# Performance work log

Hardware: AMD Instinct MI355X
Metric: run time of the kernel (lower is better)

## Reference

```python
import jax, jax.numpy as jnp
import numpy as np

HEADS = 4
PLANES = 256
IN_PLANES = 1024
W = H = D = 14
N = W * H * D  # 2744 tokens
EPS = 1e-5


def _bn_train(x, g, b):
    # training-mode BatchNorm3d: stats over (batch, spatial)
    mean = x.mean(axis=(0, 2, 3, 4), keepdims=True)
    var = ((x - mean) ** 2).mean(axis=(0, 2, 3, 4), keepdims=True)
    return g.reshape(1, -1, 1, 1, 1) * (x - mean) / jnp.sqrt(var + EPS) + b.reshape(1, -1, 1, 1, 1)


def _conv1x1(Wm, x):
    # 1x1x1 conv == channel matmul
    return jnp.einsum('oc,bcwhd->bowhd', Wm, x)


def setup_inputs() -> dict:
    key = jax.random.key(0)
    ks = jax.random.split(key, 16)
    dh = PLANES // HEADS
    s1 = 1.0 / np.sqrt(IN_PLANES)
    s2 = 1.0 / np.sqrt(PLANES)
    return {
        'x': jax.random.normal(ks[0], (4, IN_PLANES, W, H, D), jnp.float32),
        'W1': jax.random.uniform(ks[1], (PLANES, IN_PLANES), jnp.float32, -s1, s1),
        'g1': jnp.ones((PLANES,), jnp.float32),
        'b1': jnp.zeros((PLANES,), jnp.float32),
        'Wq': jax.random.uniform(ks[2], (PLANES, PLANES), jnp.float32, -s2, s2),
        'bq': jax.random.uniform(ks[3], (PLANES,), jnp.float32, -s2, s2),
        'Wk': jax.random.uniform(ks[4], (PLANES, PLANES), jnp.float32, -s2, s2),
        'bk': jax.random.uniform(ks[5], (PLANES,), jnp.float32, -s2, s2),
        'Wv': jax.random.uniform(ks[6], (PLANES, PLANES), jnp.float32, -s2, s2),
        'bv': jax.random.uniform(ks[7], (PLANES,), jnp.float32, -s2, s2),
        'rel_h': jax.random.normal(ks[8], (1, HEADS, dh, 1, H, D), jnp.float32),
        'rel_w': jax.random.normal(ks[9], (1, HEADS, dh, W, 1, D), jnp.float32),
        'rel_d': jax.random.normal(ks[10], (1, HEADS, dh, W, H, 1), jnp.float32),
        'g2': jnp.ones((PLANES,), jnp.float32),
        'b2': jnp.zeros((PLANES,), jnp.float32),
        'W3': jax.random.uniform(ks[11], (PLANES * 4, PLANES), jnp.float32, -s2, s2),
        'g3': jnp.ones((PLANES * 4,), jnp.float32),
        'b3': jnp.zeros((PLANES * 4,), jnp.float32),
    }


def _mhsa(x, Wq, bq, Wk, bk, Wv, bv, rel_h, rel_w, rel_d):
    B, C = x.shape[0], x.shape[1]
    dh = C // HEADS
    def proj(Wm, bm):
        y = _conv1x1(Wm, x) + bm.reshape(1, -1, 1, 1, 1)
        return y.reshape(B, HEADS, dh, N)
    q = proj(Wq, bq)
    k = proj(Wk, bk)
    v = proj(Wv, bv)
    # content-content: q^T k -> [B, H, N, N]
    cc = jnp.einsum('bhdn,bhdm->bhnm', q, k)
    # relative position term: (rel_h+rel_w+rel_d) broadcast to [1,H,dh,W,H,D]
    rel = (rel_h + rel_w + rel_d).reshape(HEADS, dh, N)
    cp = jnp.einsum('hdn,bhdm->bhnm', rel, q)
    attn = jax.nn.softmax(cc + cp, axis=-1)
    # out[...,n] = sum_m v[...,m] * attn[n, m]
    out = jnp.einsum('bhdm,bhnm->bhdn', v, attn)
    return out.reshape(B, C, W, H, D)


def reference(x, W1, g1, b1, Wq, bq, Wk, bk, Wv, bv, rel_h, rel_w, rel_d, g2, b2, W3, g3, b3):
    residual = x
    out = jax.nn.relu(_bn_train(_conv1x1(W1, x), g1, b1))
    out = _mhsa(out, Wq, bq, Wk, bk, Wv, bv, rel_h, rel_w, rel_d)
    out = jax.nn.relu(_bn_train(out, g2, b2))
    out = _bn_train(_conv1x1(W3, out), g3, b3)
    out = jax.nn.relu(out + residual)
    return out
```

## Files before the change

### kernel.cpp

```cpp
#include <hip/hip_runtime.h>
#include <hip/hip_bf16.h>
#include <math.h>

#define B_ 4
#define C1 1024
#define C2 256
#define HEADS_ 4
#define N_ 2744
#define NT_ 10976
#define EPS_ 1e-5f

typedef float f32x4 __attribute__((ext_vector_type(4)));
typedef short bf16x8 __attribute__((ext_vector_type(8)));
typedef unsigned short us4 __attribute__((ext_vector_type(4)));

static __device__ __forceinline__ unsigned short bfbits(float x) {
    __hip_bfloat16 t = __float2bfloat16(x);
    unsigned short u; __builtin_memcpy(&u, &t, 2); return u;
}

__global__ __launch_bounds__(256) void prep(
    const float* __restrict__ W1, const float* __restrict__ Wq, const float* __restrict__ Wk,
    const float* __restrict__ Wv, const float* __restrict__ W3,
    unsigned short* __restrict__ Wb, float* __restrict__ sums)
{
    const int bidx = blockIdx.x, t = threadIdx.x;
    if (bidx < 704) {
        const int i0 = (bidx * 256 + t) * 4;
        const float* src; int off;
        if (i0 < 262144)      { src = W1; off = i0; }
        else if (i0 < 327680) { src = Wq; off = i0 - 262144; }
        else if (i0 < 393216) { src = Wk; off = i0 - 327680; }
        else if (i0 < 458752) { src = Wv; off = i0 - 393216; }
        else                  { src = W3; off = i0 - 458752; }
        const float4 v = *(const float4*)&src[off];
        us4 pk; pk[0] = bfbits(v.x); pk[1] = bfbits(v.y); pk[2] = bfbits(v.z); pk[3] = bfbits(v.w);
        *(us4*)&Wb[i0] = pk;
    } else {
        float4 z; z.x = z.y = z.z = z.w = 0.f;
        *(float4*)&sums[t * 4] = z;
    }
}

__global__ __launch_bounds__(256) void xt_kernel(const float* __restrict__ x,
                                                 unsigned short* __restrict__ xT)
{
    __shared__ float ld[64][65];
    const int b = blockIdx.z, c0 = blockIdx.y << 6, n0 = blockIdx.x << 6;
    const int t = threadIdx.x, tn = t & 63, tg = t >> 6;
    const int gn = n0 + tn;
#pragma unroll
    for (int i = 0; i < 16; ++i) {
        const int c = tg * 16 + i;
        ld[c][tn] = (gn < N_) ? x[((size_t)b * C1 + c0 + c) * N_ + gn] : 0.f;
    }
    __syncthreads();
#pragma unroll
    for (int i = 0; i < 16; ++i) {
        const int n = tg * 16 + i;
        if (n0 + n < N_)
            xT[((size_t)b * N_ + n0 + n) * C1 + c0 + tn] = bfbits(ld[tn][n]);
    }
}

__global__ __launch_bounds__(256, 4) void gemm_nt(
    const unsigned short* __restrict__ A, const unsigned short* __restrict__ Bm,
    const float* __restrict__ bias, void* __restrict__ out0, void* __restrict__ out1,
    int M, int NC, int K, long aStride, long bStride, long oStride, int ldc, int mode)
{
    __shared__ char smem[24576];
    const int z = blockIdx.z;
    const int row0 = blockIdx.x << 7;
    const int col0 = blockIdx.y << 6;
    const unsigned short* Ag = A + (size_t)z * aStride;
    const unsigned short* Bg = Bm + (size_t)z * bStride;
    const int t = threadIdx.x;
    const int wave = t >> 6, lane = t & 63, l4 = lane >> 4, l15 = lane & 15;
    const int wr0 = wave << 5;

    f32x4 acc[2][4];
#pragma unroll
    for (int mi = 0; mi < 2; ++mi)
#pragma unroll
        for (int ks = 0; ks < 4; ++ks) acc[mi][ks] = (f32x4){0.f, 0.f, 0.f, 0.f};

    const int nk = K >> 6;
    for (int kt = 0; kt < nk; ++kt) {
        const int k0 = kt << 6;
        __syncthreads();
#pragma unroll
        for (int c = 0; c < 4; ++c) {
            const int e = c * 256 + t;
            const int r = e >> 3, ke = (e & 7) << 3;
            const int gr = min(row0 + r, M - 1);
            const bf16x8 v = *(const bf16x8*)(Ag + (size_t)gr * K + k0 + ke);
            *(bf16x8*)&smem[r * 128 + ((ke * 2) ^ ((r & 7) << 4))] = v;
        }
#pragma unroll
        for (int c = 0; c < 2; ++c) {
            const int e = c * 256 + t;
            const int r = e >> 3, ke = (e & 7) << 3;
            const int gr = min(col0 + r, NC - 1);
            const bf16x8 v = *(const bf16x8*)(Bg + (size_t)gr * K + k0 + ke);
            *(bf16x8*)&smem[16384 + r * 128 + ((ke * 2) ^ ((r & 7) << 4))] = v;
        }
        __syncthreads();
#pragma unroll
        for (int kc = 0; kc < 2; ++kc) {
            const int colb = kc * 64 + l4 * 16;
            const int ra0 = wr0 + l15, ra1 = wr0 + 16 + l15;
            const bf16x8 a0 = *(const bf16x8*)&smem[ra0 * 128 + (colb ^ ((ra0 & 7) << 4))];
            const bf16x8 a1 = *(const bf16x8*)&smem[ra1 * 128 + (colb ^ ((ra1 & 7) << 4))];
#pragma unroll
            for (int ks = 0; ks < 4; ++ks) {
                const int rb = ks * 16 + l15;
                const bf16x8 bf = *(const bf16x8*)&smem[16384 + rb * 128 + (colb ^ ((rb & 7) << 4))];
                acc[0][ks] = __builtin_amdgcn_mfma_f32_16x16x32_bf16(a0, bf, acc[0][ks], 0, 0, 0);
                acc[1][ks] = __builtin_amdgcn_mfma_f32_16x16x32_bf16(a1, bf, acc[1][ks], 0, 0, 0);
            }
        }
    }

    if (mode == 0) {
        float* o0 = (float*)out0 + (size_t)z * oStride;
#pragma unroll
        for (int mi = 0; mi < 2; ++mi)
#pragma unroll
            for (int ks = 0; ks < 4; ++ks)
#pragma unroll
                for (int j = 0; j < 4; ++j) {
                    const int row = row0 + wr0 + mi * 16 + l4 * 4 + j;
                    const int col = col0 + ks * 16 + l15;
                    if (row < M && col < NC) o0[(size_t)row * ldc + col] = acc[mi][ks][j];
                }
    } else if (mode == 3) {
        unsigned short* o0 = (unsigned short*)out0;
#pragma unroll
        for (int mi = 0; mi < 2; ++mi)
#pragma unroll
            for (int ks = 0; ks < 4; ++ks)
#pragma unroll
                for (int j = 0; j < 4; ++j) {
                    const int row = row0 + wr0 + mi * 16 + l4 * 4 + j;
                    const int col = col0 + ks * 16 + l15;
                    if (row < M && col < NC)
                        o0[((size_t)z * C2 + row) * N_ + col] = bfbits(acc[mi][ks][j] + bias[row]);
                }
    } else {
        unsigned short* yq = (unsigned short*)out0;
        unsigned short* yk = (unsigned short*)out1;
        const int h = col0 >> 6;
        const size_t bhbase = (size_t)(z * HEADS_ + h) * N_;
#pragma unroll
        for (int mi = 0; mi < 2; ++mi)
#pragma unroll
            for (int ks = 0; ks < 4; ++ks) {
                const int dcol = ks * 16 + l15;
                const float bvl = bias[col0 + dcol];
#pragma unroll
                for (int j = 0; j < 4; ++j) {
                    const int row = row0 + wr0 + mi * 16 + l4 * 4 + j;
                    if (row >= M) continue;
                    const unsigned short pv = bfbits(acc[mi][ks][j] + bvl);
                    if (mode == 1) {
                        yq[(bhbase + row) * 128 + dcol] = pv;
                        yk[(bhbase + row) * 128 + 64 + dcol] = pv;
                    } else {
                        yq[(bhbase + row) * 128 + dcol] = pv;
                    }
                }
            }
    }
}

__global__ __launch_bounds__(256) void bn_stats_t(const float* __restrict__ Y,
                                                  float* __restrict__ sums)
{
    const int c = threadIdx.x;
    float s = 0.f, s2 = 0.f;
    for (int row = blockIdx.x; row < NT_; row += gridDim.x) {
        const float v = Y[(size_t)row * 256 + c];
        s += v; s2 += v * v;
    }
    atomicAdd(&sums[c], s);
    atomicAdd(&sums[256 + c], s2);
}

__global__ __launch_bounds__(256) void bn_finalize_t(const float* __restrict__ sums,
    const float* __restrict__ g, const float* __restrict__ bb, float* __restrict__ scsh)
{
    const int c = threadIdx.x;
    const float m = sums[c] * (1.f / NT_);
    const float var = sums[256 + c] * (1.f / NT_) - m * m;
    const float istd = rsqrtf(var + EPS_);
    const float sc = g[c] * istd;
    scsh[c] = sc;
    scsh[256 + c] = bb[c] - m * sc;
}

__global__ __launch_bounds__(256) void bn_apply_t(const float* __restrict__ Y,
    const float* __restrict__ scsh, unsigned short* __restrict__ Yb)
{
    const int total4 = NT_ * 256 / 4;
    for (int i4 = blockIdx.x * 256 + threadIdx.x; i4 < total4; i4 += gridDim.x * 256) {
        const int i = i4 << 2;
        const int c0 = i & 255;
        const float4 v = *(const float4*)&Y[i];
        const float4 sc = *(const float4*)&scsh[c0];
        const float4 sh = *(const float4*)&scsh[256 + c0];
        us4 pk;
        pk[0] = bfbits(fmaxf(fmaf(v.x, sc.x, sh.x), 0.f));
        pk[1] = bfbits(fmaxf(fmaf(v.y, sc.y, sh.y), 0.f));
        pk[2] = bfbits(fmaxf(fmaf(v.z, sc.z, sh.z), 0.f));
        pk[3] = bfbits(fmaxf(fmaf(v.w, sc.w, sh.w), 0.f));
        *(us4*)&Yb[i] = pk;
    }
}

__global__ __launch_bounds__(256) void rel_fill(
    const float* __restrict__ rh, const float* __restrict__ rw, const float* __restrict__ rd,
    unsigned short* __restrict__ QAt)
{
    const int idx = blockIdx.x * 256 + threadIdx.x;
    if (idx >= HEADS_ * 16 * N_) return;
    const int n = idx % N_;
    const int t2 = idx / N_;
    const int h = t2 >> 4, dq = t2 & 15;
    const int dd = n % 14;
    const int hh = (n / 14) % 14;
    const int w = n / 196;
    us4 pk;
#pragma unroll
    for (int i = 0; i < 4; ++i) {
        const int base = (h * 64 + dq * 4 + i) * 196;
        const float v = rh[base + hh * 14 + dd]
                      + rw[base + w * 14 + dd]
                      + rd[base + w * 14 + hh];
        pk[i] = bfbits(v);
    }
#pragma unroll
    for (int b = 0; b < B_; ++b)
        *(us4*)&QAt[((size_t)(b * HEADS_ + h) * N_ + n) * 128 + 64 + dq * 4] = pk;
}

#define ALQ 0
#define ALK 32768
#define ALP 49152

__global__ __launch_bounds__(256, 2) void attn_mfma(
    const unsigned short* __restrict__ QAt, const unsigned short* __restrict__ KBt,
    const unsigned short* __restrict__ Vb, float* __restrict__ Ot)
{
    __shared__ char smem[65536];
    const int bid = blockIdx.x;
    const int sw = (bid & 7) * 44 + (bid >> 3);
    const int bh = sw / 22;
    const int ntile = sw - bh * 22;
    const int n0 = ntile << 7;
    const int b = bh >> 2, h = bh & 3;

    const unsigned short* qat = QAt + (size_t)bh * N_ * 128;
    const unsigned short* kbt = KBt + (size_t)bh * N_ * 128;
    const unsigned short* vb  = Vb + (size_t)(b * C2 + h * 64) * N_;
    float* ot = Ot + (size_t)b * N_ * 256 + h * 64;

    const int t = threadIdx.x;
    const int wave = t >> 6, lane = t & 63, l4 = lane >> 4, l15 = lane & 15;
    const int wq0 = wave << 5;

#pragma unroll
    for (int c = 0; c < 8; ++c) {
        const int o = (c * 256 + t) * 16;
        const int q = o >> 8, cb = o & 255;
        const int gq = min(n0 + q, N_ - 1);
        const bf16x8 v = *(const bf16x8*)(qat + (size_t)gq * 128 + (cb >> 1));
        *(bf16x8*)&smem[ALQ + q * 256 + (cb ^ ((q & 7) << 4))] = v;
    }

    float m_r[2][4], l_r[2][4];
    f32x4 oacc[2][4];
#pragma unroll
    for (int mi = 0; mi < 2; ++mi)
#pragma unroll
        for (int j = 0; j < 4; ++j) { m_r[mi][j] = -1e30f; l_r[mi][j] = 0.f; }
#pragma unroll
    for (int mi = 0; mi < 2; ++mi)
#pragma unroll
        for (int ds = 0; ds < 4; ++ds) oacc[mi][ds] = (f32x4){0.f, 0.f, 0.f, 0.f};

    for (int kt = 0; kt < 43; ++kt) {
        const int m0 = kt << 6;
#pragma unroll
        for (int c = 0; c < 4; ++c) {
            const int o = (c * 256 + t) * 16;
            const int r = o >> 8, cb = o & 255;
            const int gm = min(m0 + r, N_ - 1);
            const bf16x8 v = *(const bf16x8*)(kbt + (size_t)gm * 128 + (cb >> 1));
            *(bf16x8*)&smem[ALK + r * 256 + (cb ^ ((r & 7) << 4))] = v;
        }
        __syncthreads();
        bf16x8 bvr[2][4];
#pragma unroll
        for (int mc = 0; mc < 2; ++mc)
#pragma unroll
            for (int ds = 0; ds < 4; ++ds) {
                const int ms = min(m0 + mc * 32 + l4 * 8, N_ - 8);
                bvr[mc][ds] = *(const bf16x8*)(vb + (size_t)(ds * 16 + l15) * N_ + ms);
            }
        f32x4 s[2][4];
#pragma unroll
        for (int mi = 0; mi < 2; ++mi)
#pragma unroll
            for (int ks = 0; ks < 4; ++ks) s[mi][ks] = (f32x4){0.f, 0.f, 0.f, 0.f};
#pragma unroll
        for (int kc = 0; kc < 4; ++kc) {
            const int colb = kc * 64 + l4 * 16;
            const int q0r = wq0 + l15;
            const int q1r = wq0 + 16 + l15;
            const bf16x8 a0 = *(const bf16x8*)&smem[ALQ + q0r * 256 + (colb ^ ((q0r & 7) << 4))];
            const bf16x8 a1 = *(const bf16x8*)&smem[ALQ + q1r * 256 + (colb ^ ((q1r & 7) << 4))];
#pragma unroll
            for (int ks = 0; ks < 4; ++ks) {
                const int r = ks * 16 + l15;
                const bf16x8 bf = *(const bf16x8*)&smem[ALK + r * 256 + (colb ^ ((r & 7) << 4))];
                s[0][ks] = __builtin_amdgcn_mfma_f32_16x16x32_bf16(a0, bf, s[0][ks], 0, 0, 0);
                s[1][ks] = __builtin_amdgcn_mfma_f32_16x16x32_bf16(a1, bf, s[1][ks], 0, 0, 0);
            }
        }
        if (m0 + 64 > N_) {
#pragma unroll
            for (int ks = 0; ks < 4; ++ks)
                if (m0 + ks * 16 + l15 >= N_) {
                    s[0][ks] = (f32x4){-1e30f, -1e30f, -1e30f, -1e30f};
                    s[1][ks] = (f32x4){-1e30f, -1e30f, -1e30f, -1e30f};
                }
        }
        const int pbase = ALP + (wave << 12);
#pragma unroll
        for (int mi = 0; mi < 2; ++mi) {
#pragma unroll
            for (int j = 0; j < 4; ++j) {
                const float v0 = s[mi][0][j], v1 = s[mi][1][j];
                const float v2 = s[mi][2][j], v3 = s[mi][3][j];
                float rmax = fmaxf(fmaxf(v0, v1), fmaxf(v2, v3));
                rmax = fmaxf(rmax, __shfl_xor(rmax, 1, 64));
                rmax = fmaxf(rmax, __shfl_xor(rmax, 2, 64));
                rmax = fmaxf(rmax, __shfl_xor(rmax, 4, 64));
                rmax = fmaxf(rmax, __shfl_xor(rmax, 8, 64));
                const float mnew = fmaxf(m_r[mi][j], rmax);
                const float p0 = __expf(v0 - mnew), p1 = __expf(v1 - mnew);
                const float p2 = __expf(v2 - mnew), p3 = __expf(v3 - mnew);
                float ps = p0 + p1 + p2 + p3;
                ps += __shfl_xor(ps, 1, 64);
                ps += __shfl_xor(ps, 2, 64);
                ps += __shfl_xor(ps, 4, 64);
                ps += __shfl_xor(ps, 8, 64);
                const float scl = __expf(m_r[mi][j] - mnew);
                m_r[mi][j] = mnew;
                l_r[mi][j] = l_r[mi][j] * scl + ps;
                oacc[mi][0][j] *= scl; oacc[mi][1][j] *= scl;
                oacc[mi][2][j] *= scl; oacc[mi][3][j] *= scl;
                const int r = mi * 16 + l4 * 4 + j;
                const int rb = pbase + r * 128, sz = (r & 7) << 4;
                *(unsigned short*)&smem[rb + ((l15 * 2 +  0) ^ sz)] = bfbits(p0);
                *(unsigned short*)&smem[rb + ((l15 * 2 + 32) ^ sz)] = bfbits(p1);
                *(unsigned short*)&smem[rb + ((l15 * 2 + 64) ^ sz)] = bfbits(p2);
                *(unsigned short*)&smem[rb + ((l15 * 2 + 96) ^ sz)] = bfbits(p3);
            }
        }
#pragma unroll
        for (int mc = 0; mc < 2; ++mc) {
            const int colb = mc * 64 + l4 * 16;
            const int r0 = l15, r1 = 16 + l15;
            const bf16x8 pa0 = *(const bf16x8*)&smem[pbase + r0 * 128 + (colb ^ ((r0 & 7) << 4))];
            const bf16x8 pa1 = *(const bf16x8*)&smem[pbase + r1 * 128 + (colb ^ ((r1 & 7) << 4))];
#pragma unroll
            for (int ds = 0; ds < 4; ++ds) {
                oacc[0][ds] = __builtin_amdgcn_mfma_f32_16x16x32_bf16(pa0, bvr[mc][ds], oacc[0][ds], 0, 0, 0);
                oacc[1][ds] = __builtin_amdgcn_mfma_f32_16x16x32_bf16(pa1, bvr[mc][ds], oacc[1][ds], 0, 0, 0);
            }
        }
        __syncthreads();
    }

#pragma unroll
    for (int mi = 0; mi < 2; ++mi)
#pragma unroll
        for (int j = 0; j < 4; ++j) {
            const int n = n0 + wq0 + mi * 16 + l4 * 4 + j;
            if (n < N_) {
                const float inv = 1.f / l_r[mi][j];
#pragma unroll
                for (int ds = 0; ds < 4; ++ds)
                    ot[(size_t)n * 256 + ds * 16 + l15] = oacc[mi][ds][j] * inv;
            }
        }
}

__global__ __launch_bounds__(256) void bn_stats(const float* __restrict__ Y,
                                                float* __restrict__ mean, float* __restrict__ istd,
                                                int Cch)
{
    const int ch = blockIdx.x;
    float s = 0.f, s2 = 0.f;
    for (int i = threadIdx.x; i < NT_; i += 256) {
        const int b = i / N_, n = i - b * N_;
        const float v = Y[((size_t)b * Cch + ch) * N_ + n];
        s += v; s2 += v * v;
    }
#pragma unroll
    for (int off = 32; off > 0; off >>= 1) {
        s  += __shfl_down(s, off, 64);
        s2 += __shfl_down(s2, off, 64);
    }
    __shared__ float red[8];
    const int wid = threadIdx.x >> 6;
    if ((threadIdx.x & 63) == 0) { red[wid] = s; red[4 + wid] = s2; }
    __syncthreads();
    if (threadIdx.x == 0) {
        s = red[0] + red[1] + red[2] + red[3];
        s2 = red[4] + red[5] + red[6] + red[7];
        const float m = s / (float)NT_;
        const float var = s2 / (float)NT_ - m * m;
        mean[ch] = m;
        istd[ch] = rsqrtf(var + EPS_);
    }
}

__global__ __launch_bounds__(256) void bn_add_relu(float* __restrict__ Y, const float* __restrict__ X,
    const float* __restrict__ g, const float* __restrict__ bt,
    const float* __restrict__ mean, const float* __restrict__ istd)
{
    const int total4 = B_ * C1 * (N_ / 4);
    for (int i4 = blockIdx.x * 256 + threadIdx.x; i4 < total4; i4 += gridDim.x * 256) {
        const int i = i4 << 2;
        const int ch = (i / N_) % C1;
        const float sc = g[ch] * istd[ch];
        const float sh = bt[ch] - mean[ch] * sc;
        float4 y = *(float4*)&Y[i];
        const float4 x = *(const float4*)&X[i];
        y.x = fmaxf(fmaf(y.x, sc, sh) + x.x, 0.f);
        y.y = fmaxf(fmaf(y.y, sc, sh) + x.y, 0.f);
        y.z = fmaxf(fmaf(y.z, sc, sh) + x.z, 0.f);
        y.w = fmaxf(fmaf(y.w, sc, sh) + x.w, 0.f);
        *(float4*)&Y[i] = y;
    }
}

extern "C" void kernel_launch(void* const* d_in, const int* in_sizes, int n_in,
                              void* d_out, int out_size, void* d_ws, size_t ws_size,
                              hipStream_t stream)
{
    const float* x  = (const float*)d_in[0];
    const float* W1 = (const float*)d_in[1];
    const float* g1 = (const float*)d_in[2];
    const float* b1 = (const float*)d_in[3];
    const float* Wq = (const float*)d_in[4];
    const float* bq = (const float*)d_in[5];
    const float* Wk = (const float*)d_in[6];
    const float* bk = (const float*)d_in[7];
    const float* Wv = (const float*)d_in[8];
    const float* bv = (const float*)d_in[9];
    const float* rh = (const float*)d_in[10];
    const float* rw = (const float*)d_in[11];
    const float* rd = (const float*)d_in[12];
    const float* g2 = (const float*)d_in[13];
    const float* b2 = (const float*)d_in[14];
    const float* W3 = (const float*)d_in[15];
    const float* g3 = (const float*)d_in[16];
    const float* b3 = (const float*)d_in[17];
    float* out = (float*)d_out;

    float* ws = (float*)d_ws;
    unsigned short* xT  = (unsigned short*)ws;
    unsigned short* QAt = (unsigned short*)ws;
    unsigned short* KBt = (unsigned short*)(ws + 2809856);
    float* Y1t = ws + 5619712;
    float* Ot  = Y1t;
    unsigned short* Y1t16 = (unsigned short*)(ws + 8429568);
    unsigned short* Obt16 = Y1t16;
    unsigned short* Vb16 = (unsigned short*)(ws + 9834496);
    unsigned short* Wb = (unsigned short*)(ws + 11239424);
    unsigned short* W1b = Wb;
    unsigned short* Wqb = Wb + 262144;
    unsigned short* Wkb = Wb + 327680;
    unsigned short* Wvb = Wb + 393216;
    unsigned short* W3b = Wb + 458752;
    float* st = ws + 11599872;
    float* sums1 = st;
    float* sums2 = st + 512;
    float* scsh1 = st + 1024;
    float* scsh2 = st + 1536;
    float* m3 = st + 2048;
    float* i3 = st + 3072;

    dim3 blk(256);

    prep<<<dim3(705), blk, 0, stream>>>(W1, Wq, Wk, Wv, W3, Wb, sums1);
    xt_kernel<<<dim3(43, 16, B_), blk, 0, stream>>>(x, xT);

    gemm_nt<<<dim3(22, 4, B_), blk, 0, stream>>>(xT, W1b, nullptr, Y1t, nullptr,
        N_, 256, 1024, (long)N_ * 1024, 0, (long)N_ * 256, 256, 0);
    bn_stats_t<<<dim3(128), blk, 0, stream>>>(Y1t, sums1);
    bn_finalize_t<<<dim3(1), blk, 0, stream>>>(sums1, g1, b1, scsh1);
    bn_apply_t<<<dim3(1024), blk, 0, stream>>>(Y1t, scsh1, Y1t16);

    rel_fill<<<dim3((HEADS_ * 16 * N_ + 255) / 256), blk, 0, stream>>>(rh, rw, rd, QAt);

    gemm_nt<<<dim3(22, 4, B_), blk, 0, stream>>>(Y1t16, Wqb, bq, QAt, KBt,
        N_, 256, 256, (long)N_ * 256, 0, 0, 0, 1);
    gemm_nt<<<dim3(22, 4, B_), blk, 0, stream>>>(Y1t16, Wkb, bk, KBt, nullptr,
        N_, 256, 256, (long)N_ * 256, 0, 0, 0, 2);
    gemm_nt<<<dim3(2, 43, B_), blk, 0, stream>>>(Wvb, Y1t16, bv, Vb16, nullptr,
        256, N_, 256, 0, (long)N_ * 256, 0, 0, 3);

    attn_mfma<<<dim3(352), blk, 0, stream>>>(QAt, KBt, Vb16, Ot);

    bn_stats_t<<<dim3(128), blk, 0, stream>>>(Ot, sums2);
    bn_finalize_t<<<dim3(1), blk, 0, stream>>>(sums2, g2, b2, scsh2);
    bn_apply_t<<<dim3(1024), blk, 0, stream>>>(Ot, scsh2, Obt16);

    gemm_nt<<<dim3(8, 43, B_), blk, 0, stream>>>(W3b, Obt16, nullptr, out, nullptr,
        1024, N_, 256, 0, (long)N_ * 256, (long)C1 * N_, N_, 0);
    bn_stats<<<dim3(C1), blk, 0, stream>>>(out, m3, i3, C1);
    bn_add_relu<<<dim3(2048), blk, 0, stream>>>(out, x, g3, b3, m3, i3);

    (void)in_sizes; (void)n_in; (void)out_size; (void)ws_size;
}
```

Before: 497.5 us.

## Halve attention query tile to double blocks and fuse Q/K projection GEMMs

The attention kernel now processes 64 query rows per block instead of 128: each wave owns 16 rows, shared memory shrinks to 40KB and launch bounds allow 4 blocks per CU, so 688 blocks launch instead of 352. This is meant to improve occupancy and fill the 256 CUs, at the cost of each block reloading K and V tiles twice as often. Separately, the Q and K projection GEMMs are merged into a single launch over a concatenated 512-column weight, picking the bias and output buffer by column range. This removes one launch and rereads of the activation input.

```diff
diff --git a/kernel.cpp b/kernel.cpp
--- a/kernel.cpp
+++ b/kernel.cpp
@@ -65,7 +65,8 @@
 
 __global__ __launch_bounds__(256, 4) void gemm_nt(
     const unsigned short* __restrict__ A, const unsigned short* __restrict__ Bm,
-    const float* __restrict__ bias, void* __restrict__ out0, void* __restrict__ out1,
+    const float* __restrict__ bias0, const float* __restrict__ bias1,
+    void* __restrict__ out0, void* __restrict__ out1,
     int M, int NC, int K, long aStride, long bStride, long oStride, int ldc, int mode)
 {
     __shared__ char smem[24576];
@@ -144,29 +145,31 @@
                     const int row = row0 + wr0 + mi * 16 + l4 * 4 + j;
                     const int col = col0 + ks * 16 + l15;
                     if (row < M && col < NC)
-                        o0[((size_t)z * C2 + row) * N_ + col] = bfbits(acc[mi][ks][j] + bias[row]);
+                        o0[((size_t)z * C2 + row) * N_ + col] = bfbits(acc[mi][ks][j] + bias0[row]);
                 }
     } else {
         unsigned short* yq = (unsigned short*)out0;
         unsigned short* yk = (unsigned short*)out1;
-        const int h = col0 >> 6;
-        const size_t bhbase = (size_t)(z * HEADS_ + h) * N_;
+        const bool isQ = col0 < 256;
+        const int hcol = (isQ ? col0 : col0 - 256) >> 6;
+        const size_t bhbase = (size_t)(z * HEADS_ + hcol) * N_;
 #pragma unroll
         for (int mi = 0; mi < 2; ++mi)
 #pragma unroll
             for (int ks = 0; ks < 4; ++ks) {
-                const int dcol = ks * 16 + l15;
-                const float bvl = bias[col0 + dcol];
+                const int d = ks * 16 + l15;
+                const int col = col0 + d;
+                const float bvl = isQ ? bias0[col] : bias1[col - 256];
 #pragma unroll
                 for (int j = 0; j < 4; ++j) {
                     const int row = row0 + wr0 + mi * 16 + l4 * 4 + j;
                     if (row >= M) continue;
                     const unsigned short pv = bfbits(acc[mi][ks][j] + bvl);
-                    if (mode == 1) {
-                        yq[(bhbase + row) * 128 + dcol] = pv;
-                        yk[(bhbase + row) * 128 + 64 + dcol] = pv;
+                    if (isQ) {
+                        yq[(bhbase + row) * 128 + d] = pv;
+                        yk[(bhbase + row) * 128 + 64 + d] = pv;
                     } else {
-                        yq[(bhbase + row) * 128 + dcol] = pv;
+                        yk[(bhbase + row) * 128 + d] = pv;
                     }
                 }
             }
@@ -244,19 +247,19 @@
 }
 
 #define ALQ 0
-#define ALK 32768
-#define ALP 49152
-
-__global__ __launch_bounds__(256, 2) void attn_mfma(
+#define ALK 16384
+#define ALP 32768
+
+__global__ __launch_bounds__(256, 4) void attn_mfma(
     const unsigned short* __restrict__ QAt, const unsigned short* __restrict__ KBt,
     const unsigned short* __restrict__ Vb, float* __restrict__ Ot)
 {
-    __shared__ char smem[65536];
+    __shared__ char smem[40960];
     const int bid = blockIdx.x;
-    const int sw = (bid & 7) * 44 + (bid >> 3);
-    const int bh = sw / 22;
-    const int ntile = sw - bh * 22;
-    const int n0 = ntile << 7;
+    const int sw = (bid & 7) * 86 + (bid >> 3);
+    const int bh = sw / 43;
+    const int ntile = sw - bh * 43;
+    const int n0 = ntile << 6;
     const int b = bh >> 2, h = bh & 3;
 
     const unsigned short* qat = QAt + (size_t)bh * N_ * 128;
@@ -266,10 +269,10 @@
 
     const int t = threadIdx.x;
     const int wave = t >> 6, lane = t & 63, l4 = lane >> 4, l15 = lane & 15;
-    const int wq0 = wave << 5;
-
-#pragma unroll
-    for (int c = 0; c < 8; ++c) {
+    const int wq0 = wave << 4;
+
+#pragma unroll
+    for (int c = 0; c < 4; ++c) {
         const int o = (c * 256 + t) * 16;
         const int q = o >> 8, cb = o & 255;
         const int gq = min(n0 + q, N_ - 1);
@@ -277,16 +280,14 @@
         *(bf16x8*)&smem[ALQ + q * 256 + (cb ^ ((q & 7) << 4))] = v;
     }
 
-    float m_r[2][4], l_r[2][4];
-    f32x4 oacc[2][4];
-#pragma unroll
-    for (int mi = 0; mi < 2; ++mi)
-#pragma unroll
-        for (int j = 0; j < 4; ++j) { m_r[mi][j] = -1e30f; l_r[mi][j] = 0.f; }
-#pragma unroll
-    for (int mi = 0; mi < 2; ++mi)
-#pragma unroll
-        for (int ds = 0; ds < 4; ++ds) oacc[mi][ds] = (f32x4){0.f, 0.f, 0.f, 0.f};
+    float m_r[4], l_r[4];
+    f32x4 oacc[4];
+#pragma unroll
+    for (int j = 0; j < 4; ++j) { m_r[j] = -1e30f; l_r[j] = 0.f; }
+#pragma unroll
+    for (int ds = 0; ds < 4; ++ds) oacc[ds] = (f32x4){0.f, 0.f, 0.f, 0.f};
+
+    const int pbase = ALP + (wave << 11);
 
     for (int kt = 0; kt < 43; ++kt) {
         const int m0 = kt << 6;
@@ -307,94 +308,79 @@
                 const int ms = min(m0 + mc * 32 + l4 * 8, N_ - 8);
                 bvr[mc][ds] = *(const bf16x8*)(vb + (size_t)(ds * 16 + l15) * N_ + ms);
             }
-        f32x4 s[2][4];
-#pragma unroll
-        for (int mi = 0; mi < 2; ++mi)
-#pragma unroll
-            for (int ks = 0; ks < 4; ++ks) s[mi][ks] = (f32x4){0.f, 0.f, 0.f, 0.f};
+        f32x4 s[4];
+#pragma unroll
+        for (int ks = 0; ks < 4; ++ks) s[ks] = (f32x4){0.f, 0.f, 0.f, 0.f};
 #pragma unroll
         for (int kc = 0; kc < 4; ++kc) {
             const int colb = kc * 64 + l4 * 16;
-            const int q0r = wq0 + l15;
-            const int q1r = wq0 + 16 + l15;
-            const bf16x8 a0 = *(const bf16x8*)&smem[ALQ + q0r * 256 + (colb ^ ((q0r & 7) << 4))];
-            const bf16x8 a1 = *(const bf16x8*)&smem[ALQ + q1r * 256 + (colb ^ ((q1r & 7) << 4))];
+            const int qr = wq0 + l15;
+            const bf16x8 a0 = *(const bf16x8*)&smem[ALQ + qr * 256 + (colb ^ ((qr & 7) << 4))];
 #pragma unroll
             for (int ks = 0; ks < 4; ++ks) {
                 const int r = ks * 16 + l15;
                 const bf16x8 bf = *(const bf16x8*)&smem[ALK + r * 256 + (colb ^ ((r & 7) << 4))];
-                s[0][ks] = __builtin_amdgcn_mfma_f32_16x16x32_bf16(a0, bf, s[0][ks], 0, 0, 0);
-                s[1][ks] = __builtin_amdgcn_mfma_f32_16x16x32_bf16(a1, bf, s[1][ks], 0, 0, 0);
+                s[ks] = __builtin_amdgcn_mfma_f32_16x16x32_bf16(a0, bf, s[ks], 0, 0, 0);
             }
         }
         if (m0 + 64 > N_) {
 #pragma unroll
             for (int ks = 0; ks < 4; ++ks)
-                if (m0 + ks * 16 + l15 >= N_) {
-                    s[0][ks] = (f32x4){-1e30f, -1e30f, -1e30f, -1e30f};
-                    s[1][ks] = (f32x4){-1e30f, -1e30f, -1e30f, -1e30f};
-                }
-        }
-        const int pbase = ALP + (wave << 12);
-#pragma unroll
-        for (int mi = 0; mi < 2; ++mi) {
-#pragma unroll
-            for (int j = 0; j < 4; ++j) {
-                const float v0 = s[mi][0][j], v1 = s[mi][1][j];
-                const float v2 = s[mi][2][j], v3 = s[mi][3][j];
-                float rmax = fmaxf(fmaxf(v0, v1), fmaxf(v2, v3));
-                rmax = fmaxf(rmax, __shfl_xor(rmax, 1, 64));
-                rmax = fmaxf(rmax, __shfl_xor(rmax, 2, 64));
-                rmax = fmaxf(rmax, __shfl_xor(rmax, 4, 64));
-                rmax = fmaxf(rmax, __shfl_xor(rmax, 8, 64));
-                const float mnew = fmaxf(m_r[mi][j], rmax);
-                const float p0 = __expf(v0 - mnew), p1 = __expf(v1 - mnew);
-                const float p2 = __expf(v2 - mnew), p3 = __expf(v3 - mnew);
-                float ps = p0 + p1 + p2 + p3;
-                ps += __shfl_xor(ps, 1, 64);
-                ps += __shfl_xor(ps, 2, 64);
-                ps += __shfl_xor(ps, 4, 64);
-                ps += __shfl_xor(ps, 8, 64);
-                const float scl = __expf(m_r[mi][j] - mnew);
-                m_r[mi][j] = mnew;
-                l_r[mi][j] = l_r[mi][j] * scl + ps;
-                oacc[mi][0][j] *= scl; oacc[mi][1][j] *= scl;
-                oacc[mi][2][j] *= scl; oacc[mi][3][j] *= scl;
-                const int r = mi * 16 + l4 * 4 + j;
-                const int rb = pbase + r * 128, sz = (r & 7) << 4;
-                *(unsigned short*)&smem[rb + ((l15 * 2 +  0) ^ sz)] = bfbits(p0);
-                *(unsigned short*)&smem[rb + ((l15 * 2 + 32) ^ sz)] = bfbits(p1);
-                *(unsigned short*)&smem[rb + ((l15 * 2 + 64) ^ sz)] = bfbits(p2);
-                *(unsigned short*)&smem[rb + ((l15 * 2 + 96) ^ sz)] = bfbits(p3);
-            }
+                if (m0 + ks * 16 + l15 >= N_)
+                    s[ks] = (f32x4){-1e30f, -1e30f, -1e30f, -1e30f};
+        }
+#pragma unroll
+        for (int j = 0; j < 4; ++j) {
+            const float v0 = s[0][j], v1 = s[1][j];
+            const float v2 = s[2][j], v3 = s[3][j];
+            float rmax = fmaxf(fmaxf(v0, v1), fmaxf(v2, v3));
+            rmax = fmaxf(rmax, __shfl_xor(rmax, 1, 64));
+            rmax = fmaxf(rmax, __shfl_xor(rmax, 2, 64));
+            rmax = fmaxf(rmax, __shfl_xor(rmax, 4, 64));
+            rmax = fmaxf(rmax, __shfl_xor(rmax, 8, 64));
+            const float mnew = fmaxf(m_r[j], rmax);
+            const float p0 = __expf(v0 - mnew), p1 = __expf(v1 - mnew);
+            const float p2 = __expf(v2 - mnew), p3 = __expf(v3 - mnew);
+            float ps = p0 + p1 + p2 + p3;
+            ps += __shfl_xor(ps, 1, 64);
+            ps += __shfl_xor(ps, 2, 64);
+            ps += __shfl_xor(ps, 4, 64);
+            ps += __shfl_xor(ps, 8, 64);
+            const float scl = __expf(m_r[j] - mnew);
+            m_r[j] = mnew;
+            l_r[j] = l_r[j] * scl + ps;
+            oacc[0][j] *= scl; oacc[1][j] *= scl;
+            oacc[2][j] *= scl; oacc[3][j] *= scl;
+            const int r = l4 * 4 + j;
+            const int rb = pbase + r * 128, sz = (r & 7) << 4;
+            *(unsigned short*)&smem[rb + ((l15 * 2 +  0) ^ sz)] = bfbits(p0);
+            *(unsigned short*)&smem[rb + ((l15 * 2 + 32) ^ sz)] = bfbits(p1);
+            *(unsigned short*)&smem[rb + ((l15 * 2 + 64) ^ sz)] = bfbits(p2);
+            *(unsigned short*)&smem[rb + ((l15 * 2 + 96) ^ sz)] = bfbits(p3);
         }
 #pragma unroll
         for (int mc = 0; mc < 2; ++mc) {
             const int colb = mc * 64 + l4 * 16;
-            const int r0 = l15, r1 = 16 + l15;
+            const int r0 = l15;
             const bf16x8 pa0 = *(const bf16x8*)&smem[pbase + r0 * 128 + (colb ^ ((r0 & 7) << 4))];
-            const bf16x8 pa1 = *(const bf16x8*)&smem[pbase + r1 * 128 + (colb ^ ((r1 & 7) << 4))];
 #pragma unroll
             for (int ds = 0; ds < 4; ++ds) {
-                oacc[0][ds] = __builtin_amdgcn_mfma_f32_16x16x32_bf16(pa0, bvr[mc][ds], oacc[0][ds], 0, 0, 0);
-                oacc[1][ds] = __builtin_amdgcn_mfma_f32_16x16x32_bf16(pa1, bvr[mc][ds], oacc[1][ds], 0, 0, 0);
+                oacc[ds] = __builtin_amdgcn_mfma_f32_16x16x32_bf16(pa0, bvr[mc][ds], oacc[ds], 0, 0, 0);
             }
         }
         __syncthreads();
     }
 
 #pragma unroll
-    for (int mi = 0; mi < 2; ++mi)
-#pragma unroll
-        for (int j = 0; j < 4; ++j) {
-            const int n = n0 + wq0 + mi * 16 + l4 * 4 + j;
-            if (n < N_) {
-                const float inv = 1.f / l_r[mi][j];
-#pragma unroll
-                for (int ds = 0; ds < 4; ++ds)
-                    ot[(size_t)n * 256 + ds * 16 + l15] = oacc[mi][ds][j] * inv;
-            }
-        }
+    for (int j = 0; j < 4; ++j) {
+        const int n = n0 + wq0 + l4 * 4 + j;
+        if (n < N_) {
+            const float inv = 1.f / l_r[j];
+#pragma unroll
+            for (int ds = 0; ds < 4; ++ds)
+                ot[(size_t)n * 256 + ds * 16 + l15] = oacc[ds][j] * inv;
+        }
+    }
 }
 
 __global__ __launch_bounds__(256) void bn_stats(const float* __restrict__ Y,
@@ -482,8 +468,7 @@
     unsigned short* Vb16 = (unsigned short*)(ws + 9834496);
     unsigned short* Wb = (unsigned short*)(ws + 11239424);
     unsigned short* W1b = Wb;
-    unsigned short* Wqb = Wb + 262144;
-    unsigned short* Wkb = Wb + 327680;
+    unsigned short* Wqkb = Wb + 262144;
     unsigned short* Wvb = Wb + 393216;
     unsigned short* W3b = Wb + 458752;
     float* st = ws + 11599872;
@@ -499,7 +484,7 @@
     prep<<<dim3(705), blk, 0, stream>>>(W1, Wq, Wk, Wv, W3, Wb, sums1);
     xt_kernel<<<dim3(43, 16, B_), blk, 0, stream>>>(x, xT);
 
-    gemm_nt<<<dim3(22, 4, B_), blk, 0, stream>>>(xT, W1b, nullptr, Y1t, nullptr,
+    gemm_nt<<<dim3(22, 4, B_), blk, 0, stream>>>(xT, W1b, nullptr, nullptr, Y1t, nullptr,
         N_, 256, 1024, (long)N_ * 1024, 0, (long)N_ * 256, 256, 0);
     bn_stats_t<<<dim3(128), blk, 0, stream>>>(Y1t, sums1);
     bn_finalize_t<<<dim3(1), blk, 0, stream>>>(sums1, g1, b1, scsh1);
@@ -507,20 +492,18 @@
 
     rel_fill<<<dim3((HEADS_ * 16 * N_ + 255) / 256), blk, 0, stream>>>(rh, rw, rd, QAt);
 
-    gemm_nt<<<dim3(22, 4, B_), blk, 0, stream>>>(Y1t16, Wqb, bq, QAt, KBt,
-        N_, 256, 256, (long)N_ * 256, 0, 0, 0, 1);
-    gemm_nt<<<dim3(22, 4, B_), blk, 0, stream>>>(Y1t16, Wkb, bk, KBt, nullptr,
-        N_, 256, 256, (long)N_ * 256, 0, 0, 0, 2);
-    gemm_nt<<<dim3(2, 43, B_), blk, 0, stream>>>(Wvb, Y1t16, bv, Vb16, nullptr,
+    gemm_nt<<<dim3(22, 8, B_), blk, 0, stream>>>(Y1t16, Wqkb, bq, bk, QAt, KBt,
+        N_, 512, 256, (long)N_ * 256, 0, 0, 0, 1);
+    gemm_nt<<<dim3(2, 43, B_), blk, 0, stream>>>(Wvb, Y1t16, bv, nullptr, Vb16, nullptr,
         256, N_, 256, 0, (long)N_ * 256, 0, 0, 3);
 
-    attn_mfma<<<dim3(352), blk, 0, stream>>>(QAt, KBt, Vb16, Ot);
+    attn_mfma<<<dim3(688), blk, 0, stream>>>(QAt, KBt, Vb16, Ot);
 
     bn_stats_t<<<dim3(128), blk, 0, stream>>>(Ot, sums2);
     bn_finalize_t<<<dim3(1), blk, 0, stream>>>(sums2, g2, b2, scsh2);
     bn_apply_t<<<dim3(1024), blk, 0, stream>>>(Ot, scsh2, Obt16);
 
-    gemm_nt<<<dim3(8, 43, B_), blk, 0, stream>>>(W3b, Obt16, nullptr, out, nullptr,
+    gemm_nt<<<dim3(8, 43, B_), blk, 0, stream>>>(W3b, Obt16, nullptr, nullptr, out, nullptr,
         1024, N_, 256, 0, (long)N_ * 256, (long)C1 * N_, N_, 0);
     bn_stats<<<dim3(C1), blk, 0, stream>>>(out, m3, i3, C1);
     bn_add_relu<<<dim3(2048), blk, 0, stream>>>(out, x, g3, b3, m3, i3);
```

New measurement: 470.0 us. 5.5% less time.
